# Performance work log

Hardware: AMD Instinct MI355X
Metric: run time of the kernel (lower is better)

Reference implementation:

```python
import jax, jax.numpy as jnp
import numpy as np
from jax import lax

B, T, D, K = 2, 4096, 128, 256


def setup_inputs() -> dict:
    key = jax.random.key(0)
    ks = jax.random.split(key, 5)
    s = 0.05
    return {
        "z": jax.random.normal(ks[0], (B, T, D), jnp.float32),
        "conv_kernel": jax.random.normal(ks[1], (K, 1, D), jnp.float32) * s,  # flax WIO depthwise
        "conv_bias": jnp.zeros((D,), jnp.float32),
        "Wq": jax.random.normal(ks[2], (D, D), jnp.float32) * s,
        "bq": jnp.zeros((D,), jnp.float32),
        "Wk": jax.random.normal(ks[3], (D, D), jnp.float32) * s,
        "bk": jnp.zeros((D,), jnp.float32),
        "Wo": jax.random.normal(ks[4], (D, D), jnp.float32) * s,
        "bo": jnp.zeros((D,), jnp.float32),
    }


def _sphere_norm(x):
    return x / jnp.maximum(jnp.linalg.norm(x, axis=-1, keepdims=True), 1e-8)


def reference(z, conv_kernel, conv_bias, Wq, bq, Wk, bk, Wo, bo):
    Bv, Tv, Dv = z.shape
    Kv = conv_kernel.shape[0]

    # Depthwise causal memory conv (flax nn.Conv, padding='CAUSAL', groups=D)
    memory_force = lax.conv_general_dilated(
        z, conv_kernel, window_strides=(1,), padding=[(Kv - 1, 0)],
        dimension_numbers=("NWC", "WIO", "NWC"), feature_group_count=Dv,
    ) + conv_bias

    # Keys are computed from the base point z once, shared across RK4 stages
    k_hat = _sphere_norm(z @ Wk + bk)  # [B,T,D]
    mask = jnp.tril(jnp.ones((Tv, Tv), z.dtype))  # causal mask

    def vector_field(z_curr):
        q_hat = _sphere_norm(z_curr @ Wq + bq)
        dots = jnp.einsum("btd,bsd->bts", q_hat, k_hat)  # [B,T,T]
        attn = jnp.sin(dots) * mask  # Kuramoto-style sin coupling, causal
        kuramoto = jnp.einsum("bts,bsd->btd", attn, k_hat) @ Wo + bo
        total = memory_force + kuramoto
        # project to tangent space of the sphere at z_curr
        return total - jnp.sum(total * z_curr, axis=-1, keepdims=True) * z_curr

    h = 1.0

    def retract(z_base, v):
        return _sphere_norm(z_base + v)

    k1 = vector_field(z)
    k2 = vector_field(retract(z, 0.5 * h * k1))
    k3 = vector_field(retract(z, 0.5 * h * k2))
    k4 = vector_field(retract(z, h * k3))
    v_final = (h / 6.0) * (k1 + 2 * k2 + 2 * k3 + k4)
    return retract(z, v_final)
```

## Files before the change

kernel.cpp:

```cpp
#include <hip/hip_runtime.h>
#include <hip/hip_bf16.h>

#define BB 2
#define TT 4096
#define DD 128
#define KK 256
#define NROW (BB*TT)
#define NELT (NROW*DD)

typedef _Float16 f16;
typedef __attribute__((ext_vector_type(8))) f16 half8;
typedef __attribute__((ext_vector_type(2))) __fp16 fp16x2;
typedef __attribute__((ext_vector_type(4))) float f32x4;
typedef __attribute__((ext_vector_type(16))) float f32x16;
typedef __attribute__((ext_vector_type(2))) int i32x2;
typedef __attribute__((ext_vector_type(4))) int i32x4;

__device__ __forceinline__ int pack2(float a, float b){
  fp16x2 h = __builtin_amdgcn_cvt_pkrtz(a, b);
  return __builtin_bit_cast(int, h);
}

__device__ __forceinline__ void stage_w_f16(int tid, const float* __restrict__ W, f16* Wh){
  #pragma unroll
  for (int it = 0; it < 8; it++){
    int idx = tid + it*256;
    f32x4 a = *(const f32x4*)(W + (size_t)idx*8);
    f32x4 b = *(const f32x4*)(W + (size_t)idx*8 + 4);
    half8 h;
    #pragma unroll
    for (int u = 0; u < 4; u++){ h[u] = (f16)a[u]; h[4+u] = (f16)b[u]; }
    *(half8*)(Wh + (size_t)idx*8) = h;
  }
}

__device__ __forceinline__ void proj_norm_rows(
    int tid, int r0,
    const float* __restrict__ src, const float* __restrict__ W, const float* __restrict__ bias,
    f16* __restrict__ dst, f16* __restrict__ dstT)
{
  __shared__ f16 Wh[DD*DD];
  __shared__ float zs[32*DD];
  stage_w_f16(tid, W, Wh);
  #pragma unroll
  for (int it = 0; it < 4; it++){
    int idx = tid + it*256;
    *(f32x4*)(zs + idx*4) = *(const f32x4*)(src + (size_t)r0*DD + idx*4);
  }
  __syncthreads();
  int c = tid & 15, rr = tid >> 4;
  float acc0[8], acc1[8];
  #pragma unroll
  for (int u = 0; u < 8; u++){ float bv = bias[c*8+u]; acc0[u] = bv; acc1[u] = bv; }
  const float* zr0 = zs + rr*DD;
  const float* zr1 = zs + (rr+16)*DD;
  #pragma unroll 4
  for (int i = 0; i < DD; i++){
    half8 wv = *(const half8*)(Wh + i*DD + c*8);
    float a0 = zr0[i], a1 = zr1[i];
    #pragma unroll
    for (int u = 0; u < 8; u++){
      float w = (float)wv[u];
      acc0[u] = fmaf(a0, w, acc0[u]);
      acc1[u] = fmaf(a1, w, acc1[u]);
    }
  }
  float s0 = 0.f, s1 = 0.f;
  #pragma unroll
  for (int u = 0; u < 8; u++){ s0 = fmaf(acc0[u], acc0[u], s0); s1 = fmaf(acc1[u], acc1[u], s1); }
  #pragma unroll
  for (int m = 1; m < 16; m <<= 1){ s0 += __shfl_xor(s0, m, 16); s1 += __shfl_xor(s1, m, 16); }
  float inv0 = 1.f / fmaxf(sqrtf(s0), 1e-8f);
  float inv1 = 1.f / fmaxf(sqrtf(s1), 1e-8f);
  half8 h0, h1;
  #pragma unroll
  for (int u = 0; u < 8; u++){ h0[u] = (f16)(acc0[u]*inv0); h1[u] = (f16)(acc1[u]*inv1); }
  int row0 = r0 + rr, row1 = row0 + 16;
  *(half8*)(dst + (size_t)row0*DD + c*8) = h0;
  *(half8*)(dst + (size_t)row1*DD + c*8) = h1;
  if (dstT){
    int b = row0 >> 12, t0 = row0 & 4095, t1 = row1 & 4095;
    #pragma unroll
    for (int u = 0; u < 8; u++){
      dstT[((size_t)b*DD + c*8 + u)*TT + t0] = h0[u];
      dstT[((size_t)b*DD + c*8 + u)*TT + t1] = h1[u];
    }
  }
}

__global__ __launch_bounds__(256) void k_prep(
    const float* __restrict__ z, const float* __restrict__ Wk, const float* __restrict__ bk,
    const float* __restrict__ ck, const float* __restrict__ cb,
    const float* __restrict__ Wq, const float* __restrict__ bq,
    f16* __restrict__ khb, f16* __restrict__ khT, f16* __restrict__ qhb,
    float* __restrict__ mf)
{
  int tid = threadIdx.x;
  if (blockIdx.x < 512){
    int bid = blockIdx.x;
    int d = tid & 127, tg = tid >> 7;
    int b = bid >> 8;
    int tbase = ((bid & 255) << 4) + tg*8;
    const float* zb = z + (size_t)b*TT*DD;
    float acc[8];
    #pragma unroll
    for (int j = 0; j < 8; j++) acc[j] = 0.f;
    float ckq[8];
    #pragma unroll
    for (int u = 0; u < 8; u++) ckq[u] = 0.f;
    int sstart = tbase - (KK-1);
    for (int ch = 0; ch < 33; ch++){
      #pragma unroll
      for (int u = 0; u < 8; u++){
        int base = ch*8 + u;
        int s = sstart + base;
        float zv = ((unsigned)s < (unsigned)TT && base < 263) ? zb[(size_t)s*DD + d] : 0.f;
        ckq[u] = (base < KK) ? ck[(size_t)base*DD + d] : 0.f;
        #pragma unroll
        for (int j = 0; j < 8; j++) acc[j] = fmaf(ckq[(u-j)&7], zv, acc[j]);
      }
    }
    float cbv = cb[d];
    #pragma unroll
    for (int j = 0; j < 8; j++)
      mf[((size_t)b*TT + tbase + j)*DD + d] = acc[j] + cbv;
  } else if (blockIdx.x < 768){
    proj_norm_rows(tid, (blockIdx.x - 512) * 32, z, Wk, bk, khb, khT);
  } else {
    proj_norm_rows(tid, (blockIdx.x - 768) * 32, z, Wq, bq, qhb, nullptr);
  }
}

#define QTILE 128
#define NQT3 (TT/QTILE)
#define NCHUNK 144

__global__ __launch_bounds__(256,2) void k_attn17(
    const f16* __restrict__ qhb, const f16* __restrict__ khb,
    const f16* __restrict__ khT, f16* __restrict__ part)
{
  int bid = blockIdx.x;
  int b = bid / NCHUNK;
  int rem = bid - b*NCHUNK;
  int qt = 0, chunk = 0;
  #pragma unroll 1
  for (int j = NQT3-1; j >= 0; j--){
    int nch = (j + 4) >> 2;
    if (rem < nch){ qt = j; chunk = rem; break; }
    rem -= nch;
  }
  int kt0 = chunk * 8;
  int kt1 = min(kt0 + 7, 2*qt + 1);
  int t0 = qt * QTILE;

  __shared__ __align__(16) f16 KbD[2][64*136];
  __shared__ __align__(16) f16 KtD[2][128*72];

  int tid  = threadIdx.x;
  int w    = tid >> 6;
  int lane = tid & 63;
  int q31  = lane & 31;
  int hi   = lane >> 5;

  const f16* qg  = qhb + (size_t)b*TT*DD;
  const f16* kg  = khb + (size_t)b*TT*DD;
  const f16* ktg = khT + (size_t)b*DD*TT;

  int sb_r  = tid >> 4, sb_c = (tid & 15)*8;
  int st_r  = tid >> 3, st_c = (tid & 7)*8;

  int qrow_g = t0 + 32*w + q31;

  half8 qb[8];
  {
    const f16* qrow = qg + (size_t)qrow_g*DD + 8*hi;
    #pragma unroll
    for (int ks = 0; ks < 8; ks++) qb[ks] = *(const half8*)(qrow + 16*ks);
  }

  f32x16 acc[4];
  #pragma unroll
  for (int d = 0; d < 4; d++)
    #pragma unroll
    for (int i = 0; i < 16; i++) acc[d][i] = 0.f;

  half8 sKb[4], sKt[4];
  {
    int s0 = kt0 * 64;
    #pragma unroll
    for (int it = 0; it < 4; it++)
      sKb[it] = *(const half8*)(kg + (size_t)(s0 + sb_r + it*16)*DD + sb_c);
    #pragma unroll
    for (int it = 0; it < 4; it++)
      sKt[it] = *(const half8*)(ktg + (size_t)(st_r + it*32)*TT + s0 + st_c);
    #pragma unroll
    for (int it = 0; it < 4; it++)
      *(half8*)(&KbD[0][0] + (sb_r + it*16)*136 + sb_c) = sKb[it];
    #pragma unroll
    for (int it = 0; it < 4; it++)
      *(half8*)(&KtD[0][0] + (st_r + it*32)*72 + st_c) = sKt[it];
  }
  __syncthreads();

  #pragma unroll 1
  for (int kt = kt0; kt <= kt1; kt++){
    int cur = (kt - kt0) & 1;
    const f16* KbL = &KbD[cur][0];
    const f16* KtL = &KtD[cur][0];

    if (kt < kt1){
      int s0n = (kt+1) * 64;
      #pragma unroll
      for (int it = 0; it < 4; it++)
        sKb[it] = *(const half8*)(kg + (size_t)(s0n + sb_r + it*16)*DD + sb_c);
      #pragma unroll
      for (int it = 0; it < 4; it++)
        sKt[it] = *(const half8*)(ktg + (size_t)(st_r + it*32)*TT + s0n + st_c);
    }

    int s0 = kt * 64;
    f32x16 sa0, sa1;
    #pragma unroll
    for (int i = 0; i < 16; i++){ sa0[i] = 0.f; sa1[i] = 0.f; }
    #pragma unroll
    for (int ks = 0; ks < 8; ks++){
      half8 a0 = *(const half8*)(KbL + (q31)      *136 + 16*ks + 8*hi);
      half8 a1 = *(const half8*)(KbL + (32 + q31) *136 + 16*ks + 8*hi);
      sa0 = __builtin_amdgcn_mfma_f32_32x32x16_f16(a0, qb[ks], sa0, 0,0,0);
      sa1 = __builtin_amdgcn_mfma_f32_32x32x16_f16(a1, qb[ks], sa1, 0,0,0);
    }

    float p0v[16], p1v[16];
    #pragma unroll
    for (int r = 0; r < 16; r++){
      int kr = (r&3) + 8*(r>>2) + 4*hi;
      p0v[r] = (s0 + kr      <= qrow_g) ? __sinf(sa0[r]) : 0.f;
      p1v[r] = (s0 + 32 + kr <= qrow_g) ? __sinf(sa1[r]) : 0.f;
    }

    half8 pf[4];
    #pragma unroll
    for (int kb = 0; kb < 2; kb++){
      const float* pv = kb ? p1v : p0v;
      #pragma unroll
      for (int u = 0; u < 2; u++){
        int pl0 = pack2(pv[8*u+0], pv[8*u+1]);
        int pl1 = pack2(pv[8*u+2], pv[8*u+3]);
        int ph0 = pack2(pv[8*u+4], pv[8*u+5]);
        int ph1 = pack2(pv[8*u+6], pv[8*u+7]);
        int xl0 = __shfl_xor(pl0, 32);
        int xl1 = __shfl_xor(pl1, 32);
        int xh0 = __shfl_xor(ph0, 32);
        int xh1 = __shfl_xor(ph1, 32);
        i32x4 fr;
        fr[0] = hi ? xh0 : pl0;
        fr[1] = hi ? xh1 : pl1;
        fr[2] = hi ? ph0 : xl0;
        fr[3] = hi ? ph1 : xl1;
        pf[2*kb+u] = __builtin_bit_cast(half8, fr);
      }
    }

    #pragma unroll
    for (int s = 0; s < 4; s++){
      #pragma unroll
      for (int d0 = 0; d0 < 4; d0++){
        half8 bf = *(const half8*)(KtL + (32*d0 + q31)*72 + 16*s + 8*hi);
        acc[d0] = __builtin_amdgcn_mfma_f32_32x32x16_f16(pf[s], bf, acc[d0], 0,0,0);
      }
    }

    if (kt < kt1){
      f16* KbN = &KbD[cur^1][0];
      f16* KtN = &KtD[cur^1][0];
      #pragma unroll
      for (int it = 0; it < 4; it++)
        *(half8*)(KbN + (sb_r + it*16)*136 + sb_c) = sKb[it];
      #pragma unroll
      for (int it = 0; it < 4; it++)
        *(half8*)(KtN + (st_r + it*32)*72 + st_c) = sKt[it];
      __syncthreads();
    }
  }

  f16* pb = part + (size_t)bid*(QTILE*DD);
  #pragma unroll
  for (int d0 = 0; d0 < 4; d0++){
    #pragma unroll
    for (int r = 0; r < 16; r++){
      int qr = 32*w + (r&3) + 8*(r>>2) + 4*hi;
      pb[(size_t)qr*DD + 32*d0 + q31] = (f16)acc[d0][r];
    }
  }
}

__global__ __launch_bounds__(256) void k_comb2(
    const float* __restrict__ z, const float* __restrict__ Wo, const float* __restrict__ bo,
    const float* __restrict__ mf, const f16* __restrict__ part,
    const float* __restrict__ zin, float* __restrict__ zout,
    float* __restrict__ vsum, float* __restrict__ out,
    const float* __restrict__ Wq, const float* __restrict__ bq, f16* __restrict__ qhb,
    float wsum, float cretr, int first, int last)
{
  __shared__ f16 Wh[DD*DD];
  __shared__ f16 Wqh[DD*DD];
  __shared__ float As[32*DD];
  int tid = threadIdx.x;
  int r0 = blockIdx.x * 32;
  stage_w_f16(tid, Wo, Wh);
  if (!last) stage_w_f16(tid, Wq, Wqh);
  {
    int b = r0 >> 12;
    int t = r0 & 4095;
    int qt = t >> 7;
    int ro = t & 127;
    int nc = (qt + 4) >> 2;
    int base = 0;
    #pragma unroll 1
    for (int j = NQT3-1; j > qt; j--) base += (j + 4) >> 2;
    size_t sb = ((size_t)b*NCHUNK + base)*(QTILE*DD) + (size_t)ro*DD;
    #pragma unroll
    for (int it = 0; it < 2; it++){
      int idx = tid + it*256;
      const f16* s = part + sb + (size_t)idx*8;
      float a[8];
      {
        half8 v = *(const half8*)(s);
        #pragma unroll
        for (int u = 0; u < 8; u++) a[u] = (float)v[u];
      }
      for (int cc = 1; cc < nc; cc++){
        half8 v = *(const half8*)(s + (size_t)cc*(QTILE*DD));
        #pragma unroll
        for (int u = 0; u < 8; u++) a[u] += (float)v[u];
      }
      f32x4 o0v = {a[0],a[1],a[2],a[3]}, o1v = {a[4],a[5],a[6],a[7]};
      *(f32x4*)(As + idx*8) = o0v;
      *(f32x4*)(As + idx*8 + 4) = o1v;
    }
  }
  __syncthreads();
  int c = tid & 15, rr = tid >> 4;
  float kur0[8], kur1[8];
  #pragma unroll
  for (int u = 0; u < 8; u++){ float bv = bo[c*8+u]; kur0[u] = bv; kur1[u] = bv; }
  const float* ar0 = As + rr*DD;
  const float* ar1 = As + (rr+16)*DD;
  #pragma unroll 4
  for (int i = 0; i < DD; i++){
    half8 wv = *(const half8*)(Wh + i*DD + c*8);
    float a0 = ar0[i], a1 = ar1[i];
    #pragma unroll
    for (int u = 0; u < 8; u++){
      float w = (float)wv[u];
      kur0[u] = fmaf(a0, w, kur0[u]);
      kur1[u] = fmaf(a1, w, kur1[u]);
    }
  }
  size_t o0 = (size_t)(r0+rr)*DD + c*8;
  size_t o1 = (size_t)(r0+rr+16)*DD + c*8;
  float tot0[8], tot1[8], zi0[8], zi1[8];
  {
    f32x4 m0a = *(const f32x4*)(mf + o0), m0b = *(const f32x4*)(mf + o0 + 4);
    f32x4 m1a = *(const f32x4*)(mf + o1), m1b = *(const f32x4*)(mf + o1 + 4);
    f32x4 z0a = *(const f32x4*)(zin + o0), z0b = *(const f32x4*)(zin + o0 + 4);
    f32x4 z1a = *(const f32x4*)(zin + o1), z1b = *(const f32x4*)(zin + o1 + 4);
    #pragma unroll
    for (int u = 0; u < 4; u++){
      tot0[u] = m0a[u] + kur0[u]; tot0[4+u] = m0b[u] + kur0[4+u];
      tot1[u] = m1a[u] + kur1[u]; tot1[4+u] = m1b[u] + kur1[4+u];
      zi0[u] = z0a[u]; zi0[4+u] = z0b[u];
      zi1[u] = z1a[u]; zi1[4+u] = z1b[u];
    }
  }
  float p0 = 0.f, p1 = 0.f;
  #pragma unroll
  for (int u = 0; u < 8; u++){ p0 = fmaf(tot0[u], zi0[u], p0); p1 = fmaf(tot1[u], zi1[u], p1); }
  #pragma unroll
  for (int m = 1; m < 16; m <<= 1){ p0 += __shfl_xor(p0, m, 16); p1 += __shfl_xor(p1, m, 16); }
  float ki0[8], ki1[8], vs0[8], vs1[8];
  #pragma unroll
  for (int u = 0; u < 8; u++){
    ki0[u] = tot0[u] - p0 * zi0[u];
    ki1[u] = tot1[u] - p1 * zi1[u];
  }
  if (first){
    #pragma unroll
    for (int u = 0; u < 8; u++){ vs0[u] = wsum*ki0[u]; vs1[u] = wsum*ki1[u]; }
  } else {
    f32x4 v0a = *(const f32x4*)(vsum + o0), v0b = *(const f32x4*)(vsum + o0 + 4);
    f32x4 v1a = *(const f32x4*)(vsum + o1), v1b = *(const f32x4*)(vsum + o1 + 4);
    #pragma unroll
    for (int u = 0; u < 4; u++){
      vs0[u] = fmaf(wsum, ki0[u], v0a[u]); vs0[4+u] = fmaf(wsum, ki0[4+u], v0b[u]);
      vs1[u] = fmaf(wsum, ki1[u], v1a[u]); vs1[4+u] = fmaf(wsum, ki1[4+u], v1b[u]);
    }
  }
  if (!last){
    f32x4 va = {vs0[0],vs0[1],vs0[2],vs0[3]}, vb = {vs0[4],vs0[5],vs0[6],vs0[7]};
    f32x4 vc = {vs1[0],vs1[1],vs1[2],vs1[3]}, vd = {vs1[4],vs1[5],vs1[6],vs1[7]};
    *(f32x4*)(vsum + o0) = va; *(f32x4*)(vsum + o0 + 4) = vb;
    *(f32x4*)(vsum + o1) = vc; *(f32x4*)(vsum + o1 + 4) = vd;
  }
  float nz0[8], nz1[8];
  {
    f32x4 z0a = *(const f32x4*)(z + o0), z0b = *(const f32x4*)(z + o0 + 4);
    f32x4 z1a = *(const f32x4*)(z + o1), z1b = *(const f32x4*)(z + o1 + 4);
    #pragma unroll
    for (int u = 0; u < 4; u++){
      float d0a = last ? vs0[u]*(1.f/6.f)   : cretr*ki0[u];
      float d0b = last ? vs0[4+u]*(1.f/6.f) : cretr*ki0[4+u];
      float d1a = last ? vs1[u]*(1.f/6.f)   : cretr*ki1[u];
      float d1b = last ? vs1[4+u]*(1.f/6.f) : cretr*ki1[4+u];
      nz0[u] = z0a[u] + d0a; nz0[4+u] = z0b[u] + d0b;
      nz1[u] = z1a[u] + d1a; nz1[4+u] = z1b[u] + d1b;
    }
  }
  float n0 = 0.f, n1 = 0.f;
  #pragma unroll
  for (int u = 0; u < 8; u++){ n0 = fmaf(nz0[u], nz0[u], n0); n1 = fmaf(nz1[u], nz1[u], n1); }
  #pragma unroll
  for (int m = 1; m < 16; m <<= 1){ n0 += __shfl_xor(n0, m, 16); n1 += __shfl_xor(n1, m, 16); }
  float i0 = 1.f / fmaxf(sqrtf(n0), 1e-8f);
  float i1 = 1.f / fmaxf(sqrtf(n1), 1e-8f);
  float* dst = last ? out : zout;
  f32x4 ra = {nz0[0]*i0, nz0[1]*i0, nz0[2]*i0, nz0[3]*i0};
  f32x4 rb = {nz0[4]*i0, nz0[5]*i0, nz0[6]*i0, nz0[7]*i0};
  f32x4 rc = {nz1[0]*i1, nz1[1]*i1, nz1[2]*i1, nz1[3]*i1};
  f32x4 rd = {nz1[4]*i1, nz1[5]*i1, nz1[6]*i1, nz1[7]*i1};
  *(f32x4*)(dst + o0) = ra; *(f32x4*)(dst + o0 + 4) = rb;
  *(f32x4*)(dst + o1) = rc; *(f32x4*)(dst + o1 + 4) = rd;

  if (!last){
    __syncthreads();
    *(f32x4*)(As + rr*DD + c*8)          = ra;
    *(f32x4*)(As + rr*DD + c*8 + 4)      = rb;
    *(f32x4*)(As + (rr+16)*DD + c*8)     = rc;
    *(f32x4*)(As + (rr+16)*DD + c*8 + 4) = rd;
    __syncthreads();
    float q0[8], q1[8];
    #pragma unroll
    for (int u = 0; u < 8; u++){ float bv = bq[c*8+u]; q0[u] = bv; q1[u] = bv; }
    const float* qr0 = As + rr*DD;
    const float* qr1 = As + (rr+16)*DD;
    #pragma unroll 4
    for (int i = 0; i < DD; i++){
      half8 wv = *(const half8*)(Wqh + i*DD + c*8);
      float a0 = qr0[i], a1 = qr1[i];
      #pragma unroll
      for (int u = 0; u < 8; u++){
        float w = (float)wv[u];
        q0[u] = fmaf(a0, w, q0[u]);
        q1[u] = fmaf(a1, w, q1[u]);
      }
    }
    float s0 = 0.f, s1 = 0.f;
    #pragma unroll
    for (int u = 0; u < 8; u++){ s0 = fmaf(q0[u], q0[u], s0); s1 = fmaf(q1[u], q1[u], s1); }
    #pragma unroll
    for (int m = 1; m < 16; m <<= 1){ s0 += __shfl_xor(s0, m, 16); s1 += __shfl_xor(s1, m, 16); }
    float qi0 = 1.f / fmaxf(sqrtf(s0), 1e-8f);
    float qi1 = 1.f / fmaxf(sqrtf(s1), 1e-8f);
    half8 h0, h1;
    #pragma unroll
    for (int u = 0; u < 8; u++){ h0[u] = (f16)(q0[u]*qi0); h1[u] = (f16)(q1[u]*qi1); }
    *(half8*)(qhb + (size_t)(r0+rr)*DD + c*8)    = h0;
    *(half8*)(qhb + (size_t)(r0+rr+16)*DD + c*8) = h1;
  }
}

extern "C" void kernel_launch(void* const* d_in, const int* in_sizes, int n_in,
                              void* d_out, int out_size, void* d_ws, size_t ws_size,
                              hipStream_t stream) {
  const float* z  = (const float*)d_in[0];
  const float* ck = (const float*)d_in[1];
  const float* cb = (const float*)d_in[2];
  const float* Wq = (const float*)d_in[3];
  const float* bq = (const float*)d_in[4];
  const float* Wk = (const float*)d_in[5];
  const float* bk = (const float*)d_in[6];
  const float* Wo = (const float*)d_in[7];
  const float* bo = (const float*)d_in[8];
  float* out = (float*)d_out;

  float* mf   = (float*)d_ws;
  float* zc   = mf   + NELT;
  float* vsum = zc   + NELT;
  f16*   khb  = (f16*)(vsum + NELT);
  f16*   khT  = khb  + NELT;
  f16*   qhb  = khT  + NELT;
  f16*   part = qhb  + NELT;

  k_prep<<<1024, 256, 0, stream>>>(z, Wk, bk, ck, cb, Wq, bq, khb, khT, qhb, mf);

  const float wv[4] = {1.f, 2.f, 2.f, 1.f};
  const float cv[4] = {0.5f, 0.5f, 1.f, 0.f};
  for (int st = 0; st < 4; st++){
    const float* zcur = (st == 0) ? z : zc;
    k_attn17<<<BB*NCHUNK, 256, 0, stream>>>(qhb, khb, khT, part);
    k_comb2 <<<NROW/32, 256, 0, stream>>>(z, Wo, bo, mf, part, zcur, zc, vsum, out,
                                          Wq, bq, qhb, wv[st], cv[st], st == 0, st == 3);
  }
}
```

Measured before the change: 275.2 us.

## Fuse Wo projection into attention kernel epilogue via MFMA on partials

Moves the output projection by Wo from the combine kernel into the attention kernel's epilogue. Each attention block transposes Wo to fp16 in shared memory, reshuffles its accumulator into MFMA operands and multiplies the partial sums by Wo before writing them out. Because the projection is linear, the combine kernel can then just sum the partials and add the bias. This drops the scalar FMA matmul and the Wo staging from the combine kernel, at the cost of redundant Wo loads and projection work in every attention chunk block.

```diff
diff --git a/kernel.cpp b/kernel.cpp
--- a/kernel.cpp
+++ b/kernel.cpp
@@ -135,9 +135,10 @@
 #define NQT3 (TT/QTILE)
 #define NCHUNK 144
 
-__global__ __launch_bounds__(256,2) void k_attn17(
+__global__ __launch_bounds__(256,2) void k_attn18(
     const f16* __restrict__ qhb, const f16* __restrict__ khb,
-    const f16* __restrict__ khT, f16* __restrict__ part)
+    const f16* __restrict__ khT, const float* __restrict__ Wo,
+    f16* __restrict__ part)
 {
   int bid = blockIdx.x;
   int b = bid / NCHUNK;
@@ -266,7 +267,7 @@
       #pragma unroll
       for (int d0 = 0; d0 < 4; d0++){
         half8 bf = *(const half8*)(KtL + (32*d0 + q31)*72 + 16*s + 8*hi);
-        acc[d0] = __builtin_amdgcn_mfma_f32_32x32x16_f16(pf[s], bf, acc[d0], 0,0,0);
+        acc[d0] = __builtin_amdgcn_mfma_f32_32x32x16_f16(bf, pf[s], acc[d0], 0,0,0);
       }
     }
 
@@ -283,31 +284,81 @@
     }
   }
 
-  f16* pb = part + (size_t)bid*(QTILE*DD);
+  __syncthreads();
+  f16* WoT = &KbD[0][0];
+  {
+    int j  = tid & 127;
+    int ib = tid >> 7;
+    #pragma unroll
+    for (int u = 0; u < 8; u++){
+      int i0 = ib*64 + u*8;
+      half8 h;
+      #pragma unroll
+      for (int k = 0; k < 8; k++) h[k] = (f16)Wo[(size_t)(i0+k)*DD + j];
+      *(half8*)(WoT + j*136 + i0) = h;
+    }
+  }
+  half8 bO[8];
   #pragma unroll
   for (int d0 = 0; d0 < 4; d0++){
     #pragma unroll
-    for (int r = 0; r < 16; r++){
-      int qr = 32*w + (r&3) + 8*(r>>2) + 4*hi;
-      pb[(size_t)qr*DD + 32*d0 + q31] = (f16)acc[d0][r];
-    }
-  }
-}
-
-__global__ __launch_bounds__(256) void k_comb2(
-    const float* __restrict__ z, const float* __restrict__ Wo, const float* __restrict__ bo,
+    for (int m = 0; m < 2; m++){
+      int pl0 = pack2(acc[d0][8*m+0], acc[d0][8*m+1]);
+      int pl1 = pack2(acc[d0][8*m+2], acc[d0][8*m+3]);
+      int ph0 = pack2(acc[d0][8*m+4], acc[d0][8*m+5]);
+      int ph1 = pack2(acc[d0][8*m+6], acc[d0][8*m+7]);
+      int xl0 = __shfl_xor(pl0, 32);
+      int xl1 = __shfl_xor(pl1, 32);
+      int xh0 = __shfl_xor(ph0, 32);
+      int xh1 = __shfl_xor(ph1, 32);
+      i32x4 fr;
+      fr[0] = hi ? xh0 : pl0;
+      fr[1] = hi ? xh1 : pl1;
+      fr[2] = hi ? ph0 : xl0;
+      fr[3] = hi ? ph1 : xl1;
+      bO[2*d0+m] = __builtin_bit_cast(half8, fr);
+    }
+  }
+  __syncthreads();
+
+  f32x16 acc2[4];
+  #pragma unroll
+  for (int ob = 0; ob < 4; ob++)
+    #pragma unroll
+    for (int i = 0; i < 16; i++) acc2[ob][i] = 0.f;
+  #pragma unroll
+  for (int ks = 0; ks < 8; ks++){
+    #pragma unroll
+    for (int ob = 0; ob < 4; ob++){
+      half8 af = *(const half8*)(WoT + (32*ob + q31)*136 + 16*ks + 8*hi);
+      acc2[ob] = __builtin_amdgcn_mfma_f32_32x32x16_f16(af, bO[ks], acc2[ob], 0,0,0);
+    }
+  }
+
+  f16* pb = part + (size_t)bid*(QTILE*DD) + (size_t)(32*w + q31)*DD;
+  #pragma unroll
+  for (int ob = 0; ob < 4; ob++){
+    #pragma unroll
+    for (int j = 0; j < 4; j++){
+      i32x2 pw = { pack2(acc2[ob][4*j+0], acc2[ob][4*j+1]),
+                   pack2(acc2[ob][4*j+2], acc2[ob][4*j+3]) };
+      *(i32x2*)(pb + 32*ob + 8*j + 4*hi) = pw;
+    }
+  }
+}
+
+__global__ __launch_bounds__(256) void k_comb3(
+    const float* __restrict__ z, const float* __restrict__ bo,
     const float* __restrict__ mf, const f16* __restrict__ part,
     const float* __restrict__ zin, float* __restrict__ zout,
     float* __restrict__ vsum, float* __restrict__ out,
     const float* __restrict__ Wq, const float* __restrict__ bq, f16* __restrict__ qhb,
     float wsum, float cretr, int first, int last)
 {
-  __shared__ f16 Wh[DD*DD];
   __shared__ f16 Wqh[DD*DD];
   __shared__ float As[32*DD];
   int tid = threadIdx.x;
   int r0 = blockIdx.x * 32;
-  stage_w_f16(tid, Wo, Wh);
   if (!last) stage_w_f16(tid, Wq, Wqh);
   {
     int b = r0 >> 12;
@@ -342,19 +393,16 @@
   __syncthreads();
   int c = tid & 15, rr = tid >> 4;
   float kur0[8], kur1[8];
-  #pragma unroll
-  for (int u = 0; u < 8; u++){ float bv = bo[c*8+u]; kur0[u] = bv; kur1[u] = bv; }
-  const float* ar0 = As + rr*DD;
-  const float* ar1 = As + (rr+16)*DD;
-  #pragma unroll 4
-  for (int i = 0; i < DD; i++){
-    half8 wv = *(const half8*)(Wh + i*DD + c*8);
-    float a0 = ar0[i], a1 = ar1[i];
-    #pragma unroll
-    for (int u = 0; u < 8; u++){
-      float w = (float)wv[u];
-      kur0[u] = fmaf(a0, w, kur0[u]);
-      kur1[u] = fmaf(a1, w, kur1[u]);
+  {
+    f32x4 k0a = *(const f32x4*)(As + rr*DD + c*8);
+    f32x4 k0b = *(const f32x4*)(As + rr*DD + c*8 + 4);
+    f32x4 k1a = *(const f32x4*)(As + (rr+16)*DD + c*8);
+    f32x4 k1b = *(const f32x4*)(As + (rr+16)*DD + c*8 + 4);
+    #pragma unroll
+    for (int u = 0; u < 4; u++){
+      float bva = bo[c*8+u], bvb = bo[c*8+4+u];
+      kur0[u] = k0a[u] + bva; kur0[4+u] = k0b[u] + bvb;
+      kur1[u] = k1a[u] + bva; kur1[4+u] = k1b[u] + bvb;
     }
   }
   size_t o0 = (size_t)(r0+rr)*DD + c*8;
@@ -497,8 +545,8 @@
   const float cv[4] = {0.5f, 0.5f, 1.f, 0.f};
   for (int st = 0; st < 4; st++){
     const float* zcur = (st == 0) ? z : zc;
-    k_attn17<<<BB*NCHUNK, 256, 0, stream>>>(qhb, khb, khT, part);
-    k_comb2 <<<NROW/32, 256, 0, stream>>>(z, Wo, bo, mf, part, zcur, zc, vsum, out,
+    k_attn18<<<BB*NCHUNK, 256, 0, stream>>>(qhb, khb, khT, Wo, part);
+    k_comb3 <<<NROW/32, 256, 0, stream>>>(z, bo, mf, part, zcur, zc, vsum, out,
                                           Wq, bq, qhb, wv[st], cv[st], st == 0, st == 3);
   }
 }
```

Result: faster. 268.2 us (-2.5%).
